# Performance work log

Measured on AMD Instinct MI355X. Metric: run time of the kernel, lower is better.

## Reference

```python
import jax, jax.numpy as jnp
import numpy as np

H, DH, HID = 8, 16, 128
N_USER, N_ITEM, N_TASTE, N_IMAGE = 20000, 50000, 50000, 50000


def setup_inputs() -> dict:
    key = jax.random.key(0)
    ks = jax.random.split(key, 24)
    f = jax.random.normal
    s = 1.0 / np.sqrt(HID).astype(np.float32)
    inp = {
        "x_user": f(ks[0], (N_USER, HID), jnp.float32),
        "x_item": f(ks[1], (N_ITEM, HID), jnp.float32),
        "x_taste": f(ks[2], (N_TASTE, HID), jnp.float32),
        "x_image": f(ks[3], (N_IMAGE, HID), jnp.float32),
        "Wk": f(ks[4], (4, HID, HID), jnp.float32) * s,
        "bk": jnp.zeros((4, HID), jnp.float32),
        "Wq": f(ks[5], (4, HID, HID), jnp.float32) * s,
        "bq": jnp.zeros((4, HID), jnp.float32),
        "Wv": f(ks[6], (4, HID, HID), jnp.float32) * s,
        "bv": jnp.zeros((4, HID), jnp.float32),
        "a_rel": f(ks[7], (4, H, DH, DH), jnp.float32) * (1.0 / np.sqrt(DH).astype(np.float32)),
        "m_rel": f(ks[8], (4, H, DH, DH), jnp.float32) * (1.0 / np.sqrt(DH).astype(np.float32)),
        "p_rel": jnp.ones((4, H), jnp.float32),
        "Wo": f(ks[9], (2, HID, HID), jnp.float32) * s,
        "bo": jnp.zeros((2, HID), jnp.float32),
        "skip": jnp.ones((2,), jnp.float32),
        "ti_src": jax.random.randint(ks[10], (50000,), 0, N_TASTE, jnp.int32),
        "ti_dst": jax.random.randint(ks[11], (50000,), 0, N_ITEM, jnp.int32),
        "im_src": jax.random.randint(ks[12], (50000,), 0, N_IMAGE, jnp.int32),
        "im_dst": jax.random.randint(ks[13], (50000,), 0, N_ITEM, jnp.int32),
        "ub_src": jax.random.randint(ks[14], (500000,), 0, N_USER, jnp.int32),
        "ub_dst": jax.random.randint(ks[15], (500000,), 0, N_ITEM, jnp.int32),
        "bu_src": jax.random.randint(ks[16], (500000,), 0, N_ITEM, jnp.int32),
        "bu_dst": jax.random.randint(ks[17], (500000,), 0, N_USER, jnp.int32),
    }
    return inp


def _kqv(x, i, Wk, bk, Wq, bq, Wv, bv):
    k = (x @ Wk[i] + bk[i]).reshape(-1, H, DH)
    q = (x @ Wq[i] + bq[i]).reshape(-1, H, DH)
    v = (x @ Wv[i] + bv[i]).reshape(-1, H, DH)
    return k, q, v


def _edge_alpha_msg(k_src, v_src, q_dst, src, dst, a, m, p):
    # per-edge-type relation transform at node level, then gather per edge
    kr = jnp.einsum('nhd,hde->nhe', k_src, a)  # [Nsrc,H,DH]
    vr = jnp.einsum('nhd,hde->nhe', v_src, m)
    alpha = (q_dst[dst] * kr[src]).sum(-1) * p * (1.0 / np.sqrt(DH).astype(np.float32))  # [E,H]
    return alpha, vr[src]


def _seg_softmax_agg(alpha, msg, dst, n):
    amax = jax.ops.segment_max(alpha, dst, num_segments=n)
    amax = jnp.where(jnp.isfinite(amax), amax, 0.0)
    ex = jnp.exp(alpha - amax[dst])
    den = jax.ops.segment_sum(ex, dst, num_segments=n)
    w = ex / (den[dst] + 1e-16)
    return jax.ops.segment_sum(msg * w[..., None], dst, num_segments=n)  # [n,H,DH]


def reference(x_user, x_item, x_taste, x_image, Wk, bk, Wq, bq, Wv, bv,
              a_rel, m_rel, p_rel, Wo, bo, skip,
              ti_src, ti_dst, im_src, im_dst, ub_src, ub_dst, bu_src, bu_dst):
    k_u, q_u, v_u = _kqv(x_user, 0, Wk, bk, Wq, bq, Wv, bv)
    k_i, q_i, v_i = _kqv(x_item, 1, Wk, bk, Wq, bq, Wv, bv)
    k_t, _, v_t = _kqv(x_taste, 2, Wk, bk, Wq, bq, Wv, bv)
    k_g, _, v_g = _kqv(x_image, 3, Wk, bk, Wq, bq, Wv, bv)

    # edges into 'item': taste(0), image(1), user-buys(2); softmax over all combined per item
    a0, m0 = _edge_alpha_msg(k_t, v_t, q_i, ti_src, ti_dst, a_rel[0], m_rel[0], p_rel[0])
    a1, m1 = _edge_alpha_msg(k_g, v_g, q_i, im_src, im_dst, a_rel[1], m_rel[1], p_rel[1])
    a2, m2 = _edge_alpha_msg(k_u, v_u, q_i, ub_src, ub_dst, a_rel[2], m_rel[2], p_rel[2])
    alpha_i = jnp.concatenate([a0, a1, a2], 0)
    msg_i = jnp.concatenate([m0, m1, m2], 0)
    dst_i = jnp.concatenate([ti_dst, im_dst, ub_dst], 0)
    agg_i = _seg_softmax_agg(alpha_i, msg_i, dst_i, N_ITEM)

    # edges into 'user': item-bought_by(3)
    a3, m3 = _edge_alpha_msg(k_i, v_i, q_u, bu_src, bu_dst, a_rel[3], m_rel[3], p_rel[3])
    agg_u = _seg_softmax_agg(a3, m3, bu_dst, N_USER)

    out_i = jax.nn.gelu(agg_i.reshape(-1, HID), approximate=False) @ Wo[0] + bo[0]
    g_i = jax.nn.sigmoid(skip[0])
    out_i = g_i * out_i + (1.0 - g_i) * x_item

    out_u = jax.nn.gelu(agg_u.reshape(-1, HID), approximate=False) @ Wo[1] + bo[1]
    g_u = jax.nn.sigmoid(skip[1])
    out_u = g_u * out_u + (1.0 - g_u) * x_user
    return (out_i, out_u)
```

## Files before the change

### kernel.cpp

```cpp
#include <hip/hip_runtime.h>
#include <math.h>


namespace {
constexpr int HIDN  = 128;
constexpr int NHEAD = 8;

constexpr int NU = 20000, NI = 50000, NT = 50000, NG = 50000;
constexpr int E_TI = 50000, E_IM = 50000, E_UB = 500000, E_BU = 500000;
constexpr int ETOT = E_TI + E_IM + E_UB + E_BU;
constexpr int ND   = NI + NU;

constexpr int BASE_U = 0;
constexpr int BASE_I = NU;
constexpr int BASE_T = NU + NI;
constexpr int BASE_G = NU + NI + NT;

constexpr int NMAT = 12;
constexpr int MATSZ = 128 * 128;
constexpr int SU = 136;

constexpr int NBU = (NU + 63) / 64;
constexpr int NBI = (NI + 63) / 64;
constexpr int NBT = (NT + 63) / 64;
constexpr int NBG = (NG + 63) / 64;
constexpr int NPROJ = NBU + NBI + NBT + NBG;
constexpr int NBH   = (ETOT + 255) / 256;
}

typedef __attribute__((ext_vector_type(8))) short short8v;
typedef __attribute__((ext_vector_type(4))) float f32x4;
typedef __attribute__((ext_vector_type(4))) unsigned short ushort4v;

__device__ __forceinline__ unsigned short bf16rne(float f) {
    unsigned u = __float_as_uint(f);
    unsigned r = (u + 0x7fffu + ((u >> 16) & 1u)) >> 16;
    return (unsigned short)r;
}
__device__ __forceinline__ float bf16f(unsigned short h) {
    return __uint_as_float(((unsigned)h) << 16);
}
__device__ __forceinline__ float bflo(unsigned int u) { return __uint_as_float(u << 16); }
__device__ __forceinline__ float bfhi(unsigned int u) { return __uint_as_float(u & 0xffff0000u); }

__global__ void pack_kernel(const float* __restrict__ Wk, const float* __restrict__ bk,
                            const float* __restrict__ Wv, const float* __restrict__ bv,
                            const float* __restrict__ a_rel, const float* __restrict__ m_rel,
                            const float* __restrict__ p_rel,
                            const float* __restrict__ Wq, const float* __restrict__ bq,
                            const float* __restrict__ Wo, const float* __restrict__ bo,
                            short* __restrict__ pkh, short* __restrict__ pkl,
                            float* __restrict__ bias, int* __restrict__ deg)
{
    const int NW = NMAT * MATSZ;
    const int NB = NMAT * HIDN;
    int idx = blockIdx.x * blockDim.x + threadIdx.x;
    if (idx < NW) {
        int mat = idx >> 14;
        int rem = idx & (MATSZ - 1);
        int i    = rem & 7;
        int lane = (rem >> 3) & 63;
        int ct   = (rem >> 9) & 7;
        int ks   = rem >> 12;
        int k   = ks * 32 + ((lane >> 4) & 3) * 8 + i;
        int col = ct * 16 + (lane & 15);
        float v;
        if (mat < 8) {
            int which = mat >> 2;
            int tt = mat & 3;
            const int et_map[4] = {2, 3, 0, 1};
            int et = et_map[tt];
            const float* W = (which == 0 ? Wk : Wv) + (size_t)tt * MATSZ;
            const float* A = (which == 0 ? a_rel : m_rel) + (size_t)et * NHEAD * 256;
            int h = ct, e2 = col & 15;
            float s = 0.f;
#pragma unroll
            for (int d = 0; d < 16; ++d)
                s = fmaf(W[(size_t)k * HIDN + h * 16 + d], A[h * 256 + d * 16 + e2], s);
            if (which == 0) s *= p_rel[et * NHEAD + h] * 0.25f;
            v = s;
        } else if (mat < 10) {
            v = Wq[(size_t)(mat - 8) * MATSZ + (size_t)k * HIDN + col];
        } else {
            v = Wo[(size_t)(mat - 10) * MATSZ + (size_t)k * HIDN + col];
        }
        unsigned short hb = bf16rne(v);
        pkh[idx] = (short)hb;
        pkl[idx] = (short)bf16rne(v - bf16f(hb));
    } else if (idx < NW + NB) {
        int b = idx - NW;
        int mat = b >> 7, col = b & 127;
        float v;
        if (mat < 8) {
            int which = mat >> 2;
            int tt = mat & 3;
            const int et_map[4] = {2, 3, 0, 1};
            int et = et_map[tt];
            const float* bb = (which == 0 ? bk : bv) + tt * HIDN;
            const float* A  = (which == 0 ? a_rel : m_rel) + (size_t)et * NHEAD * 256;
            int h = col >> 4, e2 = col & 15;
            float s = 0.f;
#pragma unroll
            for (int d = 0; d < 16; ++d)
                s = fmaf(bb[h * 16 + d], A[h * 256 + d * 16 + e2], s);
            if (which == 0) s *= p_rel[et * NHEAD + h] * 0.25f;
            v = s;
        } else if (mat < 10) v = bq[(mat - 8) * HIDN + col];
        else                 v = bo[(mat - 10) * HIDN + col];
        bias[b] = v;
    } else if (idx < NW + NB + ND) {
        deg[idx - NW - NB] = 0;
    }
}

__global__ __launch_bounds__(256) void mfma_proj_all(
    const float* __restrict__ xu, const float* __restrict__ xi,
    const float* __restrict__ xt, const float* __restrict__ xg,
    const short* __restrict__ pkh, const short* __restrict__ pkl,
    const float* __restrict__ bias,
    unsigned short* __restrict__ krb, unsigned short* __restrict__ vrb,
    unsigned short* __restrict__ qb_u, unsigned short* __restrict__ qb_i,
    const int* __restrict__ ti_dst, const int* __restrict__ im_dst,
    const int* __restrict__ ub_dst, const int* __restrict__ bu_dst,
    int* __restrict__ deg)
{
    int b = blockIdx.x;
    if (b >= NPROJ) {
        int i = (b - NPROJ) * 256 + threadIdx.x;
        if (i < ETOT) {
            int d;
            if (i < E_TI)                     d = ti_dst[i];
            else if (i < E_TI + E_IM)         d = im_dst[i - E_TI];
            else if (i < E_TI + E_IM + E_UB)  d = ub_dst[i - E_TI - E_IM];
            else                              d = NI + bu_dst[i - E_TI - E_IM - E_UB];
            atomicAdd(&deg[d], 1);
        }
        return;
    }

    int seg, bloc;
    if (b < NBU)                  { seg = 0; bloc = b; }
    else if (b < NBU + NBI)       { seg = 1; bloc = b - NBU; }
    else if (b < NBU + NBI + NBT) { seg = 2; bloc = b - NBU - NBI; }
    else                          { seg = 3; bloc = b - NBU - NBI - NBT; }
    const float* x = (seg == 0) ? xu : (seg == 1) ? xi : (seg == 2) ? xt : xg;
    const int M     = (seg == 0) ? NU : (seg == 1) ? NI : (seg == 2) ? NT : NG;
    const int rbase = (seg == 0) ? BASE_U : (seg == 1) ? BASE_I : (seg == 2) ? BASE_T : BASE_G;
    unsigned short* qp = (seg == 0) ? qb_u : (seg == 1) ? qb_i : nullptr;

    __shared__ unsigned short hs[64 * SU];
    __shared__ unsigned short ls[64 * SU];
    const int t  = threadIdx.x;
    const int r0 = bloc * 64;
    const int rows = min(64, M - r0);

#pragma unroll
    for (int p = 0; p < 8; ++p) {
        int f = p * 256 + t;
        int row = f >> 5, c4 = f & 31;
        float4 v = make_float4(0.f, 0.f, 0.f, 0.f);
        if (row < rows) v = *(const float4*)(x + (size_t)(r0 + row) * HIDN + c4 * 4);
        float vv[4] = {v.x, v.y, v.z, v.w};
        ushort4v hq, lq;
#pragma unroll
        for (int i = 0; i < 4; ++i) {
            unsigned short hb = bf16rne(vv[i]);
            hq[i] = hb;
            lq[i] = bf16rne(vv[i] - bf16f(hb));
        }
        *(ushort4v*)&hs[row * SU + c4 * 4] = hq;
        *(ushort4v*)&ls[row * SU + c4 * 4] = lq;
    }
    __syncthreads();

    const int l = t & 63, w = t >> 6;
    const int kgrp = l >> 4;
    const int ct0  = 2 * w;
    const int ccol = l & 15;

    for (int mi = 0; mi < 3; ++mi) {
        if (mi == 2 && qp == nullptr) break;
        const int mat = (mi == 0) ? seg : (mi == 1) ? (4 + seg) : (8 + seg);
        const short8v* bh = (const short8v*)(pkh + (size_t)mat * MATSZ);
        const short8v* bl = (const short8v*)(pkl + (size_t)mat * MATSZ);
        const float*   bs = bias + mat * HIDN;

        short8v B1[4][2], B2[4][2];
#pragma unroll
        for (int ks = 0; ks < 4; ++ks) {
#pragma unroll
            for (int c = 0; c < 2; ++c) {
                B1[ks][c] = bh[(ks * 8 + ct0 + c) * 64 + l];
                if (mi == 2) B2[ks][c] = bl[(ks * 8 + ct0 + c) * 64 + l];
            }
        }

        const float bv0 = bs[(ct0 + 0) * 16 + ccol];
        const float bv1 = bs[(ct0 + 1) * 16 + ccol];

        for (int rt = 0; rt < 4; ++rt) {
            f32x4 a0, a1;
            a0[0]=0.f;a0[1]=0.f;a0[2]=0.f;a0[3]=0.f;
            a1[0]=0.f;a1[1]=0.f;a1[2]=0.f;a1[3]=0.f;
            const int arow = rt * 16 + ccol;
#pragma unroll
            for (int ks = 0; ks < 4; ++ks) {
                short8v ah = *(const short8v*)&hs[arow * SU + ks * 32 + kgrp * 8];
                short8v al = *(const short8v*)&ls[arow * SU + ks * 32 + kgrp * 8];
                a0 = __builtin_amdgcn_mfma_f32_16x16x32_bf16(ah, B1[ks][0], a0, 0, 0, 0);
                a1 = __builtin_amdgcn_mfma_f32_16x16x32_bf16(ah, B1[ks][1], a1, 0, 0, 0);
                a0 = __builtin_amdgcn_mfma_f32_16x16x32_bf16(al, B1[ks][0], a0, 0, 0, 0);
                a1 = __builtin_amdgcn_mfma_f32_16x16x32_bf16(al, B1[ks][1], a1, 0, 0, 0);
                if (mi == 2) {
                    a0 = __builtin_amdgcn_mfma_f32_16x16x32_bf16(ah, B2[ks][0], a0, 0, 0, 0);
                    a1 = __builtin_amdgcn_mfma_f32_16x16x32_bf16(ah, B2[ks][1], a1, 0, 0, 0);
                }
            }
            const int crow = r0 + rt * 16 + kgrp * 4;
            unsigned short* dst = (mi == 0) ? krb + (size_t)rbase * HIDN
                                : (mi == 1) ? vrb + (size_t)rbase * HIDN
                                            : qp;
#pragma unroll
            for (int j = 0; j < 4; ++j) {
                int grow = crow + j;
                if (grow < M) {
                    size_t o = (size_t)grow * HIDN;
                    dst[o + (ct0 + 0) * 16 + ccol] = bf16rne(a0[j] + bv0);
                    dst[o + (ct0 + 1) * 16 + ccol] = bf16rne(a1[j] + bv1);
                }
            }
        }
    }
}

__global__ __launch_bounds__(256) void mfma_out_all(
    const unsigned short* __restrict__ agg_i, const unsigned short* __restrict__ agg_u,
    const short* __restrict__ pkh, const short* __restrict__ pkl,
    const float* __restrict__ bias,
    const float* __restrict__ x_item, const float* __restrict__ x_user,
    const float* __restrict__ skip_ptr,
    float* __restrict__ outp)
{
    int b = blockIdx.x;
    int seg = (b < NBI) ? 0 : 1;
    int bloc = (seg == 0) ? b : b - NBI;
    const unsigned short* agg = (seg == 0) ? agg_i : agg_u;
    const float* xin = (seg == 0) ? x_item : x_user;
    const int M = (seg == 0) ? NI : NU;
    const int mat = 10 + seg;
    float* out = (seg == 0) ? outp : outp + (size_t)NI * HIDN;

    __shared__ unsigned short hs[64 * SU];
    __shared__ unsigned short ls[64 * SU];
    const int t  = threadIdx.x;
    const int r0 = bloc * 64;
    const int rows = min(64, M - r0);

#pragma unroll
    for (int p = 0; p < 8; ++p) {
        int f = p * 256 + t;
        int row = f >> 5, c4 = f & 31;
        float vv[4] = {0.f, 0.f, 0.f, 0.f};
        if (row < rows) {
            uint2 u = *(const uint2*)(agg + (size_t)(r0 + row) * HIDN + c4 * 4);
            vv[0] = bflo(u.x); vv[1] = bfhi(u.x);
            vv[2] = bflo(u.y); vv[3] = bfhi(u.y);
        }
        ushort4v hq, lq;
#pragma unroll
        for (int i = 0; i < 4; ++i) {
            float g = 0.5f * vv[i] * (1.0f + erff(vv[i] * 0.70710678118654752440f));
            unsigned short hb = bf16rne(g);
            hq[i] = hb;
            lq[i] = bf16rne(g - bf16f(hb));
        }
        *(ushort4v*)&hs[row * SU + c4 * 4] = hq;
        *(ushort4v*)&ls[row * SU + c4 * 4] = lq;
    }
    __syncthreads();

    const int l = t & 63, w = t >> 6;
    const int kgrp = l >> 4;
    const int ct0  = 2 * w;
    const int ccol = l & 15;

    const short8v* bh = (const short8v*)(pkh + (size_t)mat * MATSZ);
    const short8v* bl = (const short8v*)(pkl + (size_t)mat * MATSZ);
    const float*   bs = bias + mat * HIDN;

    short8v B1[4][2], B2[4][2];
#pragma unroll
    for (int ks = 0; ks < 4; ++ks) {
#pragma unroll
        for (int c = 0; c < 2; ++c) {
            B1[ks][c] = bh[(ks * 8 + ct0 + c) * 64 + l];
            B2[ks][c] = bl[(ks * 8 + ct0 + c) * 64 + l];
        }
    }

    const float gate = 1.f / (1.f + expf(-skip_ptr[seg]));
    const float og = 1.f - gate;
    const float bv0 = bs[(ct0 + 0) * 16 + ccol];
    const float bv1 = bs[(ct0 + 1) * 16 + ccol];

    for (int rt = 0; rt < 4; ++rt) {
        f32x4 a0, a1;
        a0[0]=0.f;a0[1]=0.f;a0[2]=0.f;a0[3]=0.f;
        a1[0]=0.f;a1[1]=0.f;a1[2]=0.f;a1[3]=0.f;
        const int arow = rt * 16 + ccol;
#pragma unroll
        for (int ks = 0; ks < 4; ++ks) {
            short8v ah = *(const short8v*)&hs[arow * SU + ks * 32 + kgrp * 8];
            short8v al = *(const short8v*)&ls[arow * SU + ks * 32 + kgrp * 8];
            a0 = __builtin_amdgcn_mfma_f32_16x16x32_bf16(ah, B1[ks][0], a0, 0, 0, 0);
            a1 = __builtin_amdgcn_mfma_f32_16x16x32_bf16(ah, B1[ks][1], a1, 0, 0, 0);
            a0 = __builtin_amdgcn_mfma_f32_16x16x32_bf16(al, B1[ks][0], a0, 0, 0, 0);
            a1 = __builtin_amdgcn_mfma_f32_16x16x32_bf16(al, B1[ks][1], a1, 0, 0, 0);
            a0 = __builtin_amdgcn_mfma_f32_16x16x32_bf16(ah, B2[ks][0], a0, 0, 0, 0);
            a1 = __builtin_amdgcn_mfma_f32_16x16x32_bf16(ah, B2[ks][1], a1, 0, 0, 0);
        }
        const int crow = r0 + rt * 16 + kgrp * 4;
#pragma unroll
        for (int j = 0; j < 4; ++j) {
            int grow = crow + j;
            if (grow < M) {
                size_t o = (size_t)grow * HIDN;
                size_t o0 = o + (ct0 + 0) * 16 + ccol;
                size_t o1 = o + (ct0 + 1) * 16 + ccol;
                out[o0] = gate * (a0[j] + bv0) + og * xin[o0];
                out[o1] = gate * (a1[j] + bv1) + og * xin[o1];
            }
        }
    }
}


__global__ void scan1_kernel(int* __restrict__ deg, int* __restrict__ tops, int n)
{
    __shared__ int sh[256];
    int i = blockIdx.x * 256 + threadIdx.x;
    int v = (i < n) ? deg[i] : 0;
    sh[threadIdx.x] = v;
    __syncthreads();
    for (int o = 1; o < 256; o <<= 1) {
        int t = (threadIdx.x >= o) ? sh[threadIdx.x - o] : 0;
        __syncthreads();
        sh[threadIdx.x] += t;
        __syncthreads();
    }
    if (i < n) deg[i] = sh[threadIdx.x];
    if (threadIdx.x == 255) tops[blockIdx.x] = sh[255];
}

__global__ void scan2_kernel(int* __restrict__ tops, int nb)
{
    __shared__ int sh[1024];
    int v = (threadIdx.x < nb) ? tops[threadIdx.x] : 0;
    sh[threadIdx.x] = v;
    __syncthreads();
    for (int o = 1; o < 1024; o <<= 1) {
        int t = (threadIdx.x >= o) ? sh[threadIdx.x - o] : 0;
        __syncthreads();
        sh[threadIdx.x] += t;
        __syncthreads();
    }
    if (threadIdx.x < nb) tops[threadIdx.x] = sh[threadIdx.x];
}

__global__ void scan3_kernel(const int* __restrict__ part, const int* __restrict__ tops,
                             int* __restrict__ rowptr, int* __restrict__ cursor, int n)
{
    int i = blockIdx.x * 256 + threadIdx.x;
    if (i >= n) return;
    int add = (blockIdx.x > 0) ? tops[blockIdx.x - 1] : 0;
    int prev = (i > 0) ? ((threadIdx.x > 0) ? part[i - 1] + add
                                            : ((blockIdx.x > 0) ? tops[blockIdx.x - 1] : 0))
                       : 0;
    rowptr[i + 1] = part[i] + add;
    cursor[i] = prev;
    if (i == 0) rowptr[0] = 0;
}

__global__ void scatter_kernel(const int* __restrict__ ti_src, const int* __restrict__ ti_dst,
                               const int* __restrict__ im_src, const int* __restrict__ im_dst,
                               const int* __restrict__ ub_src, const int* __restrict__ ub_dst,
                               const int* __restrict__ bu_src, const int* __restrict__ bu_dst,
                               int* __restrict__ cursor, int* __restrict__ col)
{
    int i = blockIdx.x * blockDim.x + threadIdx.x;
    if (i >= ETOT) return;
    int d, row;
    if (i < E_TI)                    { d = ti_dst[i];                  row = BASE_T + ti_src[i]; }
    else if (i < E_TI + E_IM)        { int e = i - E_TI;               row = BASE_G + im_src[e]; d = im_dst[e]; }
    else if (i < E_TI + E_IM + E_UB) { int e = i - E_TI - E_IM;        row = BASE_U + ub_src[e]; d = ub_dst[e]; }
    else                             { int e = i - E_TI - E_IM - E_UB; row = BASE_I + bu_src[e]; d = NI + bu_dst[e]; }
    int p = atomicAdd(&cursor[d], 1);
    col[p] = row;
}

__global__ __launch_bounds__(256) void f12_kernel(
    const int* __restrict__ rowptr, const int* __restrict__ rowend,
    const int* __restrict__ col,
    const unsigned int* __restrict__ krw,
    const unsigned int* __restrict__ qb_i, const unsigned int* __restrict__ qb_u,
    const unsigned int* __restrict__ vrw,
    unsigned short* __restrict__ agg_i, unsigned short* __restrict__ agg_u)
{
    int wid = (blockIdx.x << 2) + (threadIdx.x >> 6);
    if (wid >= ND) return;
    const int l = threadIdx.x & 63;

    unsigned int qu = (wid < NI) ? qb_i[(size_t)wid * 64 + l]
                                 : qb_u[(size_t)(wid - NI) * 64 + l];
    const float qx = bflo(qu), qy = bfhi(qu);

    const int start = rowptr[wid], end = rowend[wid];
    float m = -3.0e38f, ax = 0.f, ay = 0.f, den = 0.f;

    int p = start;
    for (; p + 3 < end; p += 4) {
        int r0_ = col[p], r1_ = col[p + 1], r2_ = col[p + 2], r3_ = col[p + 3];
        unsigned int u0 = krw[(size_t)r0_ * 64 + l];
        unsigned int u1 = krw[(size_t)r1_ * 64 + l];
        unsigned int u2 = krw[(size_t)r2_ * 64 + l];
        unsigned int u3 = krw[(size_t)r3_ * 64 + l];
        unsigned int v0 = vrw[(size_t)r0_ * 64 + l];
        unsigned int v1 = vrw[(size_t)r1_ * 64 + l];
        unsigned int v2 = vrw[(size_t)r2_ * 64 + l];
        unsigned int v3 = vrw[(size_t)r3_ * 64 + l];
        float d0 = qx * bflo(u0) + qy * bfhi(u0);
        float d1 = qx * bflo(u1) + qy * bfhi(u1);
        float d2 = qx * bflo(u2) + qy * bfhi(u2);
        float d3 = qx * bflo(u3) + qy * bfhi(u3);
        d0 += __shfl_xor(d0, 1); d1 += __shfl_xor(d1, 1);
        d2 += __shfl_xor(d2, 1); d3 += __shfl_xor(d3, 1);
        d0 += __shfl_xor(d0, 2); d1 += __shfl_xor(d1, 2);
        d2 += __shfl_xor(d2, 2); d3 += __shfl_xor(d3, 2);
        d0 += __shfl_xor(d0, 4); d1 += __shfl_xor(d1, 4);
        d2 += __shfl_xor(d2, 4); d3 += __shfl_xor(d3, 4);
        float mn = fmaxf(m, fmaxf(fmaxf(d0, d1), fmaxf(d2, d3)));
        float s  = __expf(m - mn);
        float e0 = __expf(d0 - mn);
        float e1 = __expf(d1 - mn);
        float e2 = __expf(d2 - mn);
        float e3 = __expf(d3 - mn);
        ax = ax * s + e0 * bflo(v0) + e1 * bflo(v1) + e2 * bflo(v2) + e3 * bflo(v3);
        ay = ay * s + e0 * bfhi(v0) + e1 * bfhi(v1) + e2 * bfhi(v2) + e3 * bfhi(v3);
        den = den * s + (e0 + e1) + (e2 + e3);
        m = mn;
    }
    for (; p < end; ++p) {
        int r0_ = col[p];
        unsigned int u0 = krw[(size_t)r0_ * 64 + l];
        unsigned int v0 = vrw[(size_t)r0_ * 64 + l];
        float d0 = qx * bflo(u0) + qy * bfhi(u0);
        d0 += __shfl_xor(d0, 1);
        d0 += __shfl_xor(d0, 2);
        d0 += __shfl_xor(d0, 4);
        float mn = fmaxf(m, d0);
        float s  = __expf(m - mn);
        float e0 = __expf(d0 - mn);
        ax = ax * s + e0 * bflo(v0);
        ay = ay * s + e0 * bfhi(v0);
        den = den * s + e0;
        m = mn;
    }

    float inv = 1.f / (den + 1e-16f);
    unsigned short* dst = (wid < NI) ? agg_i + (size_t)wid * HIDN
                                     : agg_u + (size_t)(wid - NI) * HIDN;
    unsigned int packed = (unsigned)bf16rne(ax * inv) | ((unsigned)bf16rne(ay * inv) << 16);
    *(unsigned int*)(dst + 2 * l) = packed;
}

extern "C" void kernel_launch(void* const* d_in, const int* in_sizes, int n_in,
                              void* d_out, int out_size, void* d_ws, size_t ws_size,
                              hipStream_t stream)
{
    const float* x_user = (const float*)d_in[0];
    const float* x_item = (const float*)d_in[1];
    const float* x_taste= (const float*)d_in[2];
    const float* x_image= (const float*)d_in[3];
    const float* Wk     = (const float*)d_in[4];
    const float* bk     = (const float*)d_in[5];
    const float* Wq     = (const float*)d_in[6];
    const float* bq     = (const float*)d_in[7];
    const float* Wv     = (const float*)d_in[8];
    const float* bv     = (const float*)d_in[9];
    const float* a_rel  = (const float*)d_in[10];
    const float* m_rel  = (const float*)d_in[11];
    const float* p_rel  = (const float*)d_in[12];
    const float* Wo     = (const float*)d_in[13];
    const float* bo     = (const float*)d_in[14];
    const float* skip   = (const float*)d_in[15];
    const int* ti_src = (const int*)d_in[16];
    const int* ti_dst = (const int*)d_in[17];
    const int* im_src = (const int*)d_in[18];
    const int* im_dst = (const int*)d_in[19];
    const int* ub_src = (const int*)d_in[20];
    const int* ub_dst = (const int*)d_in[21];
    const int* bu_src = (const int*)d_in[22];
    const int* bu_dst = (const int*)d_in[23];

    float* ws = (float*)d_ws;
    float* outp = (float*)d_out;
    (void)in_sizes; (void)n_in; (void)out_size;

    size_t off = 0;
    auto alloc = [&](size_t n) { size_t o = off; off += n; return o; };
    const size_t o_pkh  = alloc((size_t)NMAT * MATSZ / 2);
    const size_t o_pkl  = alloc((size_t)NMAT * MATSZ / 2);
    const size_t o_bias = alloc((size_t)NMAT * HIDN);
    const size_t o_krb  = alloc((size_t)(NU + NI + NT + NG) * HIDN / 2);
    const size_t o_vrb  = alloc((size_t)(NU + NI + NT + NG) * HIDN / 2);
    const size_t o_q_i  = alloc((size_t)NI * HIDN / 2);
    const size_t o_q_u  = alloc((size_t)NU * HIDN / 2);
    const size_t o_agg  = alloc((size_t)(NI + NU) * HIDN / 2);
    const size_t o_int  = alloc((size_t)(ND + 1) + ND + 1024 + ETOT + ND);

    if (ws_size < off * sizeof(float)) return;

    unsigned short* krb  = (unsigned short*)(ws + o_krb);
    unsigned short* vrb  = (unsigned short*)(ws + o_vrb);
    unsigned short* qb_i = (unsigned short*)(ws + o_q_i);
    unsigned short* qb_u = (unsigned short*)(ws + o_q_u);

    short* pkh  = (short*)(ws + o_pkh);
    short* pkl  = (short*)(ws + o_pkl);
    float* bias = ws + o_bias;

    int* rowptr = (int*)(ws + o_int);
    int* cursor = rowptr + (ND + 1);
    int* tops   = cursor + ND;
    int* col    = tops + 1024;
    int* deg    = col + ETOT;

    unsigned short* agg_i = (unsigned short*)(ws + o_agg);
    unsigned short* agg_u = agg_i + (size_t)NI * HIDN;

    {
        int ptotal = NMAT * MATSZ + NMAT * HIDN + ND;
        pack_kernel<<<(ptotal + 255) / 256, 256, 0, stream>>>(
            Wk, bk, Wv, bv, a_rel, m_rel, p_rel, Wq, bq, Wo, bo,
            pkh, pkl, bias, deg);
    }

    mfma_proj_all<<<NPROJ + NBH, 256, 0, stream>>>(
        x_user, x_item, x_taste, x_image, pkh, pkl, bias,
        krb, vrb, qb_u, qb_i,
        ti_dst, im_dst, ub_dst, bu_dst, deg);

    const int NB1 = (ND + 255) / 256;
    scan1_kernel<<<NB1, 256, 0, stream>>>(deg, tops, ND);
    scan2_kernel<<<1, 1024, 0, stream>>>(tops, NB1);
    scan3_kernel<<<NB1, 256, 0, stream>>>(deg, tops, rowptr, cursor, ND);
    scatter_kernel<<<(ETOT + 255) / 256, 256, 0, stream>>>(
        ti_src, ti_dst, im_src, im_dst, ub_src, ub_dst, bu_src, bu_dst, cursor, col);

    const int NBW = (ND + 3) / 4;
    f12_kernel<<<NBW, 256, 0, stream>>>(
        rowptr, cursor, col,
        (const unsigned int*)krb, (const unsigned int*)qb_i, (const unsigned int*)qb_u,
        (const unsigned int*)vrb,
        agg_i, agg_u);

    mfma_out_all<<<NBI + NBU, 256, 0, stream>>>(
        agg_i, agg_u, pkh, pkl, bias, x_item, x_user, skip, outp);
}
```

Before: 299.0 us.

## Interleave K and V rows into one buffer and split degree histogram kernel

The projected K and V for each source node now go into a single interleaved buffer: each pair of bf16 K values sits next to the matching pair of V values. The edge aggregation kernel can then fetch both with one 8-byte load per edge instead of two separate 4-byte loads from different arrays. This is meant to cut scattered memory transactions in the gather-heavy softmax kernel. The degree histogram moves out of the projection kernel into its own launch, which adds one kernel launch but removes the branching tail blocks from the projection grid. The projection stores become strided 2-byte writes across the interleaved layout, which may write less efficiently.

```diff
diff --git a/kernel.cpp b/kernel.cpp
--- a/kernel.cpp
+++ b/kernel.cpp
@@ -25,7 +25,6 @@
 constexpr int NBT = (NT + 63) / 64;
 constexpr int NBG = (NG + 63) / 64;
 constexpr int NPROJ = NBU + NBI + NBT + NBG;
-constexpr int NBH   = (ETOT + 255) / 256;
 }
 
 typedef __attribute__((ext_vector_type(8))) short short8v;
@@ -118,26 +117,10 @@
     const float* __restrict__ xt, const float* __restrict__ xg,
     const short* __restrict__ pkh, const short* __restrict__ pkl,
     const float* __restrict__ bias,
-    unsigned short* __restrict__ krb, unsigned short* __restrict__ vrb,
-    unsigned short* __restrict__ qb_u, unsigned short* __restrict__ qb_i,
-    const int* __restrict__ ti_dst, const int* __restrict__ im_dst,
-    const int* __restrict__ ub_dst, const int* __restrict__ bu_dst,
-    int* __restrict__ deg)
+    unsigned short* __restrict__ kvb,
+    unsigned short* __restrict__ qb_u, unsigned short* __restrict__ qb_i)
 {
     int b = blockIdx.x;
-    if (b >= NPROJ) {
-        int i = (b - NPROJ) * 256 + threadIdx.x;
-        if (i < ETOT) {
-            int d;
-            if (i < E_TI)                     d = ti_dst[i];
-            else if (i < E_TI + E_IM)         d = im_dst[i - E_TI];
-            else if (i < E_TI + E_IM + E_UB)  d = ub_dst[i - E_TI - E_IM];
-            else                              d = NI + bu_dst[i - E_TI - E_IM - E_UB];
-            atomicAdd(&deg[d], 1);
-        }
-        return;
-    }
-
     int seg, bloc;
     if (b < NBU)                  { seg = 0; bloc = b; }
     else if (b < NBU + NBI)       { seg = 1; bloc = b - NBU; }
@@ -217,16 +200,30 @@
                 }
             }
             const int crow = r0 + rt * 16 + kgrp * 4;
-            unsigned short* dst = (mi == 0) ? krb + (size_t)rbase * HIDN
-                                : (mi == 1) ? vrb + (size_t)rbase * HIDN
-                                            : qp;
-#pragma unroll
-            for (int j = 0; j < 4; ++j) {
-                int grow = crow + j;
-                if (grow < M) {
-                    size_t o = (size_t)grow * HIDN;
-                    dst[o + (ct0 + 0) * 16 + ccol] = bf16rne(a0[j] + bv0);
-                    dst[o + (ct0 + 1) * 16 + ccol] = bf16rne(a1[j] + bv1);
+            if (mi < 2) {
+                const int side = (mi == 0) ? 0 : 2;
+                const int c0 = (ct0 + 0) * 16 + ccol;
+                const int c1 = (ct0 + 1) * 16 + ccol;
+                const int i0 = 4 * (c0 >> 1) + side + (c0 & 1);
+                const int i1 = 4 * (c1 >> 1) + side + (c1 & 1);
+#pragma unroll
+                for (int j = 0; j < 4; ++j) {
+                    int grow = crow + j;
+                    if (grow < M) {
+                        size_t base = (size_t)(rbase + grow) * 256;
+                        kvb[base + i0] = bf16rne(a0[j] + bv0);
+                        kvb[base + i1] = bf16rne(a1[j] + bv1);
+                    }
+                }
+            } else {
+#pragma unroll
+                for (int j = 0; j < 4; ++j) {
+                    int grow = crow + j;
+                    if (grow < M) {
+                        size_t o = (size_t)grow * HIDN;
+                        qp[o + (ct0 + 0) * 16 + ccol] = bf16rne(a0[j] + bv0);
+                        qp[o + (ct0 + 1) * 16 + ccol] = bf16rne(a1[j] + bv1);
+                    }
                 }
             }
         }
@@ -334,6 +331,20 @@
     }
 }
 
+
+__global__ void hist_kernel(const int* __restrict__ ti_dst, const int* __restrict__ im_dst,
+                            const int* __restrict__ ub_dst, const int* __restrict__ bu_dst,
+                            int* __restrict__ deg)
+{
+    int i = blockIdx.x * blockDim.x + threadIdx.x;
+    if (i >= ETOT) return;
+    int d;
+    if (i < E_TI)                     d = ti_dst[i];
+    else if (i < E_TI + E_IM)         d = im_dst[i - E_TI];
+    else if (i < E_TI + E_IM + E_UB)  d = ub_dst[i - E_TI - E_IM];
+    else                              d = NI + bu_dst[i - E_TI - E_IM - E_UB];
+    atomicAdd(&deg[d], 1);
+}
 
 __global__ void scan1_kernel(int* __restrict__ deg, int* __restrict__ tops, int n)
 {
@@ -401,9 +412,8 @@
 __global__ __launch_bounds__(256) void f12_kernel(
     const int* __restrict__ rowptr, const int* __restrict__ rowend,
     const int* __restrict__ col,
-    const unsigned int* __restrict__ krw,
+    const unsigned int* __restrict__ kvw,
     const unsigned int* __restrict__ qb_i, const unsigned int* __restrict__ qb_u,
-    const unsigned int* __restrict__ vrw,
     unsigned short* __restrict__ agg_i, unsigned short* __restrict__ agg_u)
 {
     int wid = (blockIdx.x << 2) + (threadIdx.x >> 6);
@@ -420,18 +430,14 @@
     int p = start;
     for (; p + 3 < end; p += 4) {
         int r0_ = col[p], r1_ = col[p + 1], r2_ = col[p + 2], r3_ = col[p + 3];
-        unsigned int u0 = krw[(size_t)r0_ * 64 + l];
-        unsigned int u1 = krw[(size_t)r1_ * 64 + l];
-        unsigned int u2 = krw[(size_t)r2_ * 64 + l];
-        unsigned int u3 = krw[(size_t)r3_ * 64 + l];
-        unsigned int v0 = vrw[(size_t)r0_ * 64 + l];
-        unsigned int v1 = vrw[(size_t)r1_ * 64 + l];
-        unsigned int v2 = vrw[(size_t)r2_ * 64 + l];
-        unsigned int v3 = vrw[(size_t)r3_ * 64 + l];
-        float d0 = qx * bflo(u0) + qy * bfhi(u0);
-        float d1 = qx * bflo(u1) + qy * bfhi(u1);
-        float d2 = qx * bflo(u2) + qy * bfhi(u2);
-        float d3 = qx * bflo(u3) + qy * bfhi(u3);
+        uint2 kv0 = *(const uint2*)(kvw + (size_t)r0_ * 128 + 2 * l);
+        uint2 kv1 = *(const uint2*)(kvw + (size_t)r1_ * 128 + 2 * l);
+        uint2 kv2 = *(const uint2*)(kvw + (size_t)r2_ * 128 + 2 * l);
+        uint2 kv3 = *(const uint2*)(kvw + (size_t)r3_ * 128 + 2 * l);
+        float d0 = qx * bflo(kv0.x) + qy * bfhi(kv0.x);
+        float d1 = qx * bflo(kv1.x) + qy * bfhi(kv1.x);
+        float d2 = qx * bflo(kv2.x) + qy * bfhi(kv2.x);
+        float d3 = qx * bflo(kv3.x) + qy * bfhi(kv3.x);
         d0 += __shfl_xor(d0, 1); d1 += __shfl_xor(d1, 1);
         d2 += __shfl_xor(d2, 1); d3 += __shfl_xor(d3, 1);
         d0 += __shfl_xor(d0, 2); d1 += __shfl_xor(d1, 2);
@@ -444,24 +450,23 @@
         float e1 = __expf(d1 - mn);
         float e2 = __expf(d2 - mn);
         float e3 = __expf(d3 - mn);
-        ax = ax * s + e0 * bflo(v0) + e1 * bflo(v1) + e2 * bflo(v2) + e3 * bflo(v3);
-        ay = ay * s + e0 * bfhi(v0) + e1 * bfhi(v1) + e2 * bfhi(v2) + e3 * bfhi(v3);
+        ax = ax * s + e0 * bflo(kv0.y) + e1 * bflo(kv1.y) + e2 * bflo(kv2.y) + e3 * bflo(kv3.y);
+        ay = ay * s + e0 * bfhi(kv0.y) + e1 * bfhi(kv1.y) + e2 * bfhi(kv2.y) + e3 * bfhi(kv3.y);
         den = den * s + (e0 + e1) + (e2 + e3);
         m = mn;
     }
     for (; p < end; ++p) {
         int r0_ = col[p];
-        unsigned int u0 = krw[(size_t)r0_ * 64 + l];
-        unsigned int v0 = vrw[(size_t)r0_ * 64 + l];
-        float d0 = qx * bflo(u0) + qy * bfhi(u0);
+        uint2 kv0 = *(const uint2*)(kvw + (size_t)r0_ * 128 + 2 * l);
+        float d0 = qx * bflo(kv0.x) + qy * bfhi(kv0.x);
         d0 += __shfl_xor(d0, 1);
         d0 += __shfl_xor(d0, 2);
         d0 += __shfl_xor(d0, 4);
         float mn = fmaxf(m, d0);
         float s  = __expf(m - mn);
         float e0 = __expf(d0 - mn);
-        ax = ax * s + e0 * bflo(v0);
-        ay = ay * s + e0 * bfhi(v0);
+        ax = ax * s + e0 * bflo(kv0.y);
+        ay = ay * s + e0 * bfhi(kv0.y);
         den = den * s + e0;
         m = mn;
     }
@@ -511,8 +516,7 @@
     const size_t o_pkh  = alloc((size_t)NMAT * MATSZ / 2);
     const size_t o_pkl  = alloc((size_t)NMAT * MATSZ / 2);
     const size_t o_bias = alloc((size_t)NMAT * HIDN);
-    const size_t o_krb  = alloc((size_t)(NU + NI + NT + NG) * HIDN / 2);
-    const size_t o_vrb  = alloc((size_t)(NU + NI + NT + NG) * HIDN / 2);
+    const size_t o_kvb  = alloc((size_t)(NU + NI + NT + NG) * HIDN);
     const size_t o_q_i  = alloc((size_t)NI * HIDN / 2);
     const size_t o_q_u  = alloc((size_t)NU * HIDN / 2);
     const size_t o_agg  = alloc((size_t)(NI + NU) * HIDN / 2);
@@ -520,8 +524,7 @@
 
     if (ws_size < off * sizeof(float)) return;
 
-    unsigned short* krb  = (unsigned short*)(ws + o_krb);
-    unsigned short* vrb  = (unsigned short*)(ws + o_vrb);
+    unsigned short* kvb  = (unsigned short*)(ws + o_kvb);
     unsigned short* qb_i = (unsigned short*)(ws + o_q_i);
     unsigned short* qb_u = (unsigned short*)(ws + o_q_u);
 
@@ -545,11 +548,11 @@
             pkh, pkl, bias, deg);
     }
 
-    mfma_proj_all<<<NPROJ + NBH, 256, 0, stream>>>(
+    mfma_proj_all<<<NPROJ, 256, 0, stream>>>(
         x_user, x_item, x_taste, x_image, pkh, pkl, bias,
-        krb, vrb, qb_u, qb_i,
-        ti_dst, im_dst, ub_dst, bu_dst, deg);
-
+        kvb, qb_u, qb_i);
+
+    hist_kernel<<<(ETOT + 255) / 256, 256, 0, stream>>>(ti_dst, im_dst, ub_dst, bu_dst, deg);
     const int NB1 = (ND + 255) / 256;
     scan1_kernel<<<NB1, 256, 0, stream>>>(deg, tops, ND);
     scan2_kernel<<<1, 1024, 0, stream>>>(tops, NB1);
@@ -560,8 +563,7 @@
     const int NBW = (ND + 3) / 4;
     f12_kernel<<<NBW, 256, 0, stream>>>(
         rowptr, cursor, col,
-        (const unsigned int*)krb, (const unsigned int*)qb_i, (const unsigned int*)qb_u,
-        (const unsigned int*)vrb,
+        (const unsigned int*)kvb, (const unsigned int*)qb_i, (const unsigned int*)qb_u,
         agg_i, agg_u);
 
     mfma_out_all<<<NBI + NBU, 256, 0, stream>>>(
```

Result: slower. 311.5 us (+4.2%).
